# Optimization experiments

Measured on AMD Instinct MI355X. Metric: run time of the kernel, lower is better.

## Reference

```python
import jax, jax.numpy as jnp
import numpy as np

N = 10000
K = 32
D_GROUP = 256  # per-group input features
OUT_DIM = 256


def setup_inputs() -> dict:
    key = jax.random.key(0)
    ks = jax.random.split(key, 6)
    x = jax.random.normal(ks[0], (N, 2 * D_GROUP), dtype=jnp.float32)
    W1 = jax.random.normal(ks[1], (OUT_DIM, D_GROUP), dtype=jnp.float32) / np.sqrt(D_GROUP)
    a1 = jax.random.uniform(ks[2], (OUT_DIM,), dtype=jnp.float32)
    W2 = jax.random.normal(ks[3], (OUT_DIM, D_GROUP), dtype=jnp.float32) / np.sqrt(D_GROUP)
    a2 = jax.random.uniform(ks[4], (OUT_DIM,), dtype=jnp.float32)
    graph = jax.random.randint(ks[5], (N, K), 0, N)  # precomputed kNN indices
    return {"x": x, "W1": W1, "a1": a1, "W2": W2, "a2": a2, "graph": graph}


def _gat_layer(xg, W, a, graph):
    # linear transform: (N, out_dim)
    out = xg @ W.T
    # rescale by softmax feature weights (gaussian kernel, rescale=True)
    fw = jax.nn.softmax(a)
    out = out * fw
    # nonlinearity_1 = Hardtanh
    out = jnp.clip(out, -1.0, 1.0)
    # gather k-NN features: (N, K, out_dim)
    neigh = out[graph]
    # gaussian attention score over neighbors: (N, K)
    att = -jnp.sum((out[:, None, :] - neigh) ** 2, axis=-1)
    att = jax.nn.softmax(att, axis=-1)
    # weighted neighbor aggregation: (N, out_dim)
    return jnp.einsum("nk,nkd->nd", att, neigh)


def reference(x, W1, a1, W2, a2, graph):
    y1 = _gat_layer(x[:, :D_GROUP], W1, a1, graph)
    y2 = _gat_layer(x[:, D_GROUP:], W2, a2, graph)
    # merge=False -> concatenate group outputs
    return jnp.concatenate([y1, y2], axis=-1)
```

## Files before the change

### kernel.cpp

```cpp
#include <hip/hip_runtime.h>
#include <math.h>

#define N_NODES 10000
#define K_NB    32
#define D       256
#define XD      512

typedef __attribute__((ext_vector_type(8))) short  short8;
typedef __attribute__((ext_vector_type(4))) float  f32x4;

typedef __attribute__((address_space(1))) const unsigned int g_u32;
typedef __attribute__((address_space(3))) unsigned int       l_u32;

__device__ __forceinline__ void gld_lds16(const void* g, void* l) {
    __builtin_amdgcn_global_load_lds((g_u32*)g, (l_u32*)l, 16, 0, 0);
}

__device__ __forceinline__ float clip1(float v) { return fminf(fmaxf(v, -1.f), 1.f); }

__device__ __forceinline__ unsigned int bf16_rne(float f) {
    unsigned int u = __float_as_uint(f);
    return (u + 0x7FFFu + ((u >> 16) & 1u)) >> 16;
}
__device__ __forceinline__ float bf16f(unsigned int h) { return __uint_as_float(h << 16); }
__device__ __forceinline__ float blo(unsigned int u) { return __uint_as_float(u << 16); }
__device__ __forceinline__ float bhif(unsigned int u) { return __uint_as_float(u & 0xFFFF0000u); }

__device__ __forceinline__ void cvt8(float4 A, float4 B, uint4& hi, uint4& lo) {
    const float v[8] = {A.x, A.y, A.z, A.w, B.x, B.y, B.z, B.w};
    unsigned int h[8], q[8];
    #pragma unroll
    for (int i = 0; i < 8; ++i) {
        h[i] = bf16_rne(v[i]);
        q[i] = bf16_rne(v[i] - bf16f(h[i]));
    }
    hi = make_uint4(h[0] | (h[1] << 16), h[2] | (h[3] << 16),
                    h[4] | (h[5] << 16), h[6] | (h[7] << 16));
    lo = make_uint4(q[0] | (q[1] << 16), q[2] | (q[3] << 16),
                    q[4] | (q[5] << 16), q[6] | (q[7] << 16));
}

__global__ __launch_bounds__(256)
void conv_w(const float* __restrict__ W1, const float* __restrict__ W2,
            unsigned short* __restrict__ Whi, unsigned short* __restrict__ Wlo)
{
    const int u    = blockIdx.x * 256 + threadIdx.x;
    const int gidx = u >> 13;
    const int rem  = u & 8191;
    const float* __restrict__ W = gidx ? W2 : W1;
    const float4 f0 = *(const float4*)&W[rem * 8];
    const float4 f1 = *(const float4*)&W[rem * 8 + 4];
    uint4 hi, lo;
    cvt8(f0, f1, hi, lo);
    *(uint4*)&Whi[gidx * 65536 + rem * 8] = hi;
    *(uint4*)&Wlo[gidx * 65536 + rem * 8] = lo;
}

__global__ __launch_bounds__(256, 6)
void gemm_mfma(const float* __restrict__ x,
               const float* __restrict__ a1, const float* __restrict__ a2,
               const unsigned short* __restrict__ Whi,
               const unsigned short* __restrict__ Wlo,
               unsigned short* __restrict__ t16)
{
    const int slab = blockIdx.x;
    const int cz   = blockIdx.y;
    const int g    = blockIdx.z;
    const float* __restrict__ a = g ? a2 : a1;
    const int tid = threadIdx.x;
    const int w   = tid >> 6;
    const int l   = tid & 63;

    __shared__ float          As[32 * 32];
    __shared__ unsigned short Bhs[128 * 32];
    __shared__ unsigned short Bls[128 * 32];
    __shared__ float fwL[D];
    __shared__ float red[16];

    {
        float v = a[tid];
        float m = v;
        #pragma unroll
        for (int o = 32; o; o >>= 1) m = fmaxf(m, __shfl_xor(m, o));
        if ((tid & 63) == 0) red[tid >> 6] = m;
        __syncthreads();
        m = fmaxf(fmaxf(red[0], red[1]), fmaxf(red[2], red[3]));
        float e = expf(v - m);
        float s = e;
        #pragma unroll
        for (int o = 32; o; o >>= 1) s += __shfl_xor(s, o);
        if ((tid & 63) == 0) red[4 + (tid >> 6)] = s;
        __syncthreads();
        s = red[4] + red[5] + red[6] + red[7];
        fwL[tid] = e / s;
    }
    __syncthreads();

    const unsigned short* __restrict__ WhiG = Whi + (g << 16);
    const unsigned short* __restrict__ WloG = Wlo + (g << 16);

    const int arloc = tid >> 3;
    int agrow = slab * 32 + arloc;
    if (agrow > N_NODES - 1) agrow = N_NODES - 1;
    const int akg   = (tid & 7) ^ (arloc & 7);
    const float* aSrcBase = &x[(size_t)agrow * XD + g * D + akg * 4];

    const int brloc0 = tid >> 2;
    const int brloc1 = brloc0 + 64;
    const int bkg0   = (tid & 3) ^ ((brloc0 >> 1) & 3);
    const int bkg1   = (tid & 3) ^ ((brloc1 >> 1) & 3);
    const unsigned short* bhSrc0 = &WhiG[(cz * 128 + brloc0) * 256 + bkg0 * 8];
    const unsigned short* bhSrc1 = &WhiG[(cz * 128 + brloc1) * 256 + bkg1 * 8];
    const unsigned short* blSrc0 = &WloG[(cz * 128 + brloc0) * 256 + bkg0 * 8];
    const unsigned short* blSrc1 = &WloG[(cz * 128 + brloc1) * 256 + bkg1 * 8];

    const int woff = (tid >> 6) * 1024;

    f32x4 acc[4];
    #pragma unroll
    for (int i = 0; i < 4; ++i) acc[i] = (f32x4){0.f, 0.f, 0.f, 0.f};

    const int arow_l = 16 * (w >> 1) + (l & 15);
    const int s      = l >> 4;
    const int ct0    = (w & 1) * 4;

    for (int kc = 0; kc < 8; ++kc) {
        gld_lds16(aSrcBase + kc * 32,  (char*)As  + woff);
        gld_lds16(bhSrc0   + kc * 32,  (char*)Bhs + woff);
        gld_lds16(bhSrc1   + kc * 32,  (char*)Bhs + 4096 + woff);
        gld_lds16(blSrc0   + kc * 32,  (char*)Bls + woff);
        gld_lds16(blSrc1   + kc * 32,  (char*)Bls + 4096 + woff);
        __syncthreads();

        const int kg0 = (2 * s)     ^ (arow_l & 7);
        const int kg1 = (2 * s + 1) ^ (arow_l & 7);
        const float4 xa = *(const float4*)((const char*)As + arow_l * 128 + kg0 * 16);
        const float4 xb = *(const float4*)((const char*)As + arow_l * 128 + kg1 * 16);
        uint4 ahi, alo;
        cvt8(xa, xb, ahi, alo);
        const short8 ah = __builtin_bit_cast(short8, ahi);
        const short8 al = __builtin_bit_cast(short8, alo);

        #pragma unroll
        for (int i = 0; i < 4; ++i) {
            const int brow_l = (ct0 + i) * 16 + (l & 15);
            const int bkg    = s ^ ((brow_l >> 1) & 3);
            const short8 bh = __builtin_bit_cast(short8,
                *(const uint4*)((const char*)Bhs + brow_l * 64 + bkg * 16));
            const short8 bl = __builtin_bit_cast(short8,
                *(const uint4*)((const char*)Bls + brow_l * 64 + bkg * 16));
            acc[i] = __builtin_amdgcn_mfma_f32_16x16x32_bf16(ah, bh, acc[i], 0, 0, 0);
            acc[i] = __builtin_amdgcn_mfma_f32_16x16x32_bf16(al, bh, acc[i], 0, 0, 0);
            acc[i] = __builtin_amdgcn_mfma_f32_16x16x32_bf16(ah, bl, acc[i], 0, 0, 0);
        }
        __syncthreads();
    }

    #pragma unroll
    for (int i = 0; i < 4; ++i) {
        const int   col = cz * 128 + (ct0 + i) * 16 + (l & 15);
        const float fw  = fwL[col];
        #pragma unroll
        for (int r = 0; r < 4; ++r) {
            const int row = slab * 32 + 16 * (w >> 1) + (l >> 4) * 4 + r;
            if (row < N_NODES)
                t16[(size_t)row * XD + g * D + col] =
                    (unsigned short)bf16_rne(clip1(acc[i][r] * fw));
        }
    }
}

__global__ __launch_bounds__(256, 8)
void gat_aggregate(const unsigned short* __restrict__ t16,
                   const int* __restrict__ graph, float* __restrict__ out)
{
    const int n   = blockIdx.x;
    const int g   = blockIdx.y;
    const int tid = threadIdx.x;
    const int w   = tid >> 6;
    const int l   = tid & 63;

    __shared__ float part[4][D];
    __shared__ float Ssh[4];

    int rows[8];
    #pragma unroll
    for (int kk = 0; kk < 8; ++kk)
        rows[kk] = graph[(size_t)n * K_NB + (w + kk * 4)];

    const size_t gcol = (size_t)g * D + 4 * l;
    const uint2 ov = *(const uint2*)&t16[(size_t)n * XD + gcol];
    const float o0 = blo(ov.x), o1 = bhif(ov.x), o2 = blo(ov.y), o3 = bhif(ov.y);

    uint2 nbu[8];
    #pragma unroll
    for (int kk = 0; kk < 8; ++kk)
        nbu[kk] = *(const uint2*)&t16[(size_t)rows[kk] * XD + gcol];

    float nf[8][4];
    float d2p[8];
    #pragma unroll
    for (int kk = 0; kk < 8; ++kk) {
        nf[kk][0] = blo(nbu[kk].x); nf[kk][1] = bhif(nbu[kk].x);
        nf[kk][2] = blo(nbu[kk].y); nf[kk][3] = bhif(nbu[kk].y);
        const float dx = o0 - nf[kk][0], dy = o1 - nf[kk][1];
        const float dz = o2 - nf[kk][2], dw = o3 - nf[kk][3];
        d2p[kk] = dx * dx + dy * dy + dz * dz + dw * dw;
    }

    const bool b0 = l & 1, b1 = l & 2, b2 = l & 4;
    float u[4];
    #pragma unroll
    for (int i = 0; i < 4; ++i) {
        const float give = b0 ? d2p[2 * i] : d2p[2 * i + 1];
        const float keep = b0 ? d2p[2 * i + 1] : d2p[2 * i];
        u[i] = keep + __shfl_xor(give, 1);
    }
    float v[2];
    #pragma unroll
    for (int i = 0; i < 2; ++i) {
        const float give = b1 ? u[2 * i] : u[2 * i + 1];
        const float keep = b1 ? u[2 * i + 1] : u[2 * i];
        v[i] = keep + __shfl_xor(give, 2);
    }
    float d2 = (b2 ? v[1] : v[0]) + __shfl_xor(b2 ? v[0] : v[1], 4);
    d2 += __shfl_xor(d2, 8);
    d2 += __shfl_xor(d2, 16);
    d2 += __shfl_xor(d2, 32);

    const float e = __expf(-d2);

    float Sw = e;
    Sw += __shfl_xor(Sw, 1);
    Sw += __shfl_xor(Sw, 2);
    Sw += __shfl_xor(Sw, 4);

    const int base = l & 56;
    float4 p = make_float4(0.f, 0.f, 0.f, 0.f);
    #pragma unroll
    for (int kk = 0; kk < 8; ++kk) {
        const float ak = __shfl(e, base + kk);
        p.x += ak * nf[kk][0]; p.y += ak * nf[kk][1];
        p.z += ak * nf[kk][2]; p.w += ak * nf[kk][3];
    }

    *(float4*)&part[w][4 * l] = p;
    if (l == 0) Ssh[w] = Sw;
    __syncthreads();

    const float rS = 1.f / (Ssh[0] + Ssh[1] + Ssh[2] + Ssh[3]);
    const float y  = (part[0][tid] + part[1][tid] + part[2][tid] + part[3][tid]) * rS;
    out[(size_t)n * XD + (size_t)g * D + tid] = y;
}

extern "C" void kernel_launch(void* const* d_in, const int* in_sizes, int n_in,
                              void* d_out, int out_size, void* d_ws, size_t ws_size,
                              hipStream_t stream) {
    const float* x     = (const float*)d_in[0];
    const float* W1    = (const float*)d_in[1];
    const float* a1    = (const float*)d_in[2];
    const float* W2    = (const float*)d_in[3];
    const float* a2    = (const float*)d_in[4];
    const int*   graph = (const int*)d_in[5];
    float* out = (float*)d_out;

    unsigned short* t16 = (unsigned short*)d_ws;
    unsigned short* Whi = t16 + (size_t)N_NODES * XD;
    unsigned short* Wlo = Whi + 2 * 65536;

    conv_w<<<64, 256, 0, stream>>>(W1, W2, Whi, Wlo);

    dim3 grid1(313, 2, 2);
    gemm_mfma<<<grid1, 256, 0, stream>>>(x, a1, a2, Whi, Wlo, t16);

    dim3 grid2(N_NODES, 2);
    gat_aggregate<<<grid2, 256, 0, stream>>>(t16, graph, out);
}
```

Baseline: 126.7 us.

## Double-buffer GEMM LDS tiles and prefetch the first stage before the softmax prologue

Doubles the shared-memory A/B tiles in the MFMA GEMM so the next k-chunk's global-to-LDS loads are issued before computing on the current chunk. This leaves one barrier per iteration instead of two. The first stage is issued before the feature-weight softmax prologue so its latency hides behind that work. The loop is fully unrolled and the occupancy hint is lowered from 6 to 3 blocks, trading occupancy for overlap. The doubled LDS footprint reduces resident blocks, and the compiler's wait placement for async LDS loads may limit the overlap.

```diff
diff --git a/kernel.cpp b/kernel.cpp
--- a/kernel.cpp
+++ b/kernel.cpp
@@ -56,7 +56,7 @@
     *(uint4*)&Wlo[gidx * 65536 + rem * 8] = lo;
 }
 
-__global__ __launch_bounds__(256, 6)
+__global__ __launch_bounds__(256, 3)
 void gemm_mfma(const float* __restrict__ x,
                const float* __restrict__ a1, const float* __restrict__ a2,
                const unsigned short* __restrict__ Whi,
@@ -71,30 +71,11 @@
     const int w   = tid >> 6;
     const int l   = tid & 63;
 
-    __shared__ float          As[32 * 32];
-    __shared__ unsigned short Bhs[128 * 32];
-    __shared__ unsigned short Bls[128 * 32];
+    __shared__ float          As[2][32 * 32];
+    __shared__ unsigned short Bhs[2][128 * 32];
+    __shared__ unsigned short Bls[2][128 * 32];
     __shared__ float fwL[D];
     __shared__ float red[16];
-
-    {
-        float v = a[tid];
-        float m = v;
-        #pragma unroll
-        for (int o = 32; o; o >>= 1) m = fmaxf(m, __shfl_xor(m, o));
-        if ((tid & 63) == 0) red[tid >> 6] = m;
-        __syncthreads();
-        m = fmaxf(fmaxf(red[0], red[1]), fmaxf(red[2], red[3]));
-        float e = expf(v - m);
-        float s = e;
-        #pragma unroll
-        for (int o = 32; o; o >>= 1) s += __shfl_xor(s, o);
-        if ((tid & 63) == 0) red[4 + (tid >> 6)] = s;
-        __syncthreads();
-        s = red[4] + red[5] + red[6] + red[7];
-        fwL[tid] = e / s;
-    }
-    __syncthreads();
 
     const unsigned short* __restrict__ WhiG = Whi + (g << 16);
     const unsigned short* __restrict__ WloG = Wlo + (g << 16);
@@ -114,7 +95,37 @@
     const unsigned short* blSrc0 = &WloG[(cz * 128 + brloc0) * 256 + bkg0 * 8];
     const unsigned short* blSrc1 = &WloG[(cz * 128 + brloc1) * 256 + bkg1 * 8];
 
-    const int woff = (tid >> 6) * 1024;
+    const int woff = w * 1024;
+
+    #define STAGE(buf, kc)                                                     \
+        do {                                                                   \
+            gld_lds16(aSrcBase + (kc) * 32, (char*)As[buf]  + woff);           \
+            gld_lds16(bhSrc0   + (kc) * 32, (char*)Bhs[buf] + woff);           \
+            gld_lds16(bhSrc1   + (kc) * 32, (char*)Bhs[buf] + 4096 + woff);    \
+            gld_lds16(blSrc0   + (kc) * 32, (char*)Bls[buf] + woff);           \
+            gld_lds16(blSrc1   + (kc) * 32, (char*)Bls[buf] + 4096 + woff);    \
+        } while (0)
+
+    STAGE(0, 0);
+
+    {
+        float v = a[tid];
+        float m = v;
+        #pragma unroll
+        for (int o = 32; o; o >>= 1) m = fmaxf(m, __shfl_xor(m, o));
+        if ((tid & 63) == 0) red[tid >> 6] = m;
+        __syncthreads();
+        m = fmaxf(fmaxf(red[0], red[1]), fmaxf(red[2], red[3]));
+        float e = expf(v - m);
+        float s = e;
+        #pragma unroll
+        for (int o = 32; o; o >>= 1) s += __shfl_xor(s, o);
+        if ((tid & 63) == 0) red[4 + (tid >> 6)] = s;
+        __syncthreads();
+        s = red[4] + red[5] + red[6] + red[7];
+        fwL[tid] = e / s;
+    }
+    __syncthreads();
 
     f32x4 acc[4];
     #pragma unroll
@@ -124,18 +135,15 @@
     const int s      = l >> 4;
     const int ct0    = (w & 1) * 4;
 
+    #pragma unroll
     for (int kc = 0; kc < 8; ++kc) {
-        gld_lds16(aSrcBase + kc * 32,  (char*)As  + woff);
-        gld_lds16(bhSrc0   + kc * 32,  (char*)Bhs + woff);
-        gld_lds16(bhSrc1   + kc * 32,  (char*)Bhs + 4096 + woff);
-        gld_lds16(blSrc0   + kc * 32,  (char*)Bls + woff);
-        gld_lds16(blSrc1   + kc * 32,  (char*)Bls + 4096 + woff);
-        __syncthreads();
+        const int cur = kc & 1;
+        if (kc < 7) STAGE(cur ^ 1, kc + 1);
 
         const int kg0 = (2 * s)     ^ (arow_l & 7);
         const int kg1 = (2 * s + 1) ^ (arow_l & 7);
-        const float4 xa = *(const float4*)((const char*)As + arow_l * 128 + kg0 * 16);
-        const float4 xb = *(const float4*)((const char*)As + arow_l * 128 + kg1 * 16);
+        const float4 xa = *(const float4*)((const char*)As[cur] + arow_l * 128 + kg0 * 16);
+        const float4 xb = *(const float4*)((const char*)As[cur] + arow_l * 128 + kg1 * 16);
         uint4 ahi, alo;
         cvt8(xa, xb, ahi, alo);
         const short8 ah = __builtin_bit_cast(short8, ahi);
@@ -146,15 +154,16 @@
             const int brow_l = (ct0 + i) * 16 + (l & 15);
             const int bkg    = s ^ ((brow_l >> 1) & 3);
             const short8 bh = __builtin_bit_cast(short8,
-                *(const uint4*)((const char*)Bhs + brow_l * 64 + bkg * 16));
+                *(const uint4*)((const char*)Bhs[cur] + brow_l * 64 + bkg * 16));
             const short8 bl = __builtin_bit_cast(short8,
-                *(const uint4*)((const char*)Bls + brow_l * 64 + bkg * 16));
+                *(const uint4*)((const char*)Bls[cur] + brow_l * 64 + bkg * 16));
             acc[i] = __builtin_amdgcn_mfma_f32_16x16x32_bf16(ah, bh, acc[i], 0, 0, 0);
             acc[i] = __builtin_amdgcn_mfma_f32_16x16x32_bf16(al, bh, acc[i], 0, 0, 0);
             acc[i] = __builtin_amdgcn_mfma_f32_16x16x32_bf16(ah, bl, acc[i], 0, 0, 0);
         }
         __syncthreads();
     }
+    #undef STAGE
 
     #pragma unroll
     for (int i = 0; i < 4; ++i) {
```

Result: no change. 128.7 us (+1.6%).
